# Kernel optimization log

Hardware: AMD Instinct MI355X
Metric: run time of the kernel (lower is better)

The kernel has to match this reference:

```python
import jax, jax.numpy as jnp
import numpy as np

H = 1024      # hidden_size
V = 32000     # output_size (vocab)
L = 512       # max_length (encoder positions)
B = 256       # batch


def setup_inputs() -> dict:
    key = jax.random.key(0)
    ks = jax.random.split(key, 12)
    s = 0.02
    return {
        "input": jax.random.randint(ks[0], (B,), 0, V),
        "hidden": jax.random.normal(ks[1], (1, B, H), jnp.float32),
        "encoder_outputs": jax.random.normal(ks[2], (L, H), jnp.float32),
        # learned params (PyTorch layout: Linear weight is [out, in])
        "emb": jax.random.normal(ks[3], (V, H), jnp.float32) * s,
        "attn_W": jax.random.normal(ks[4], (L, 2 * H), jnp.float32) * s,
        "attn_b": jnp.zeros((L,), jnp.float32),
        "comb_W": jax.random.normal(ks[5], (H, 2 * H), jnp.float32) * s,
        "comb_b": jnp.zeros((H,), jnp.float32),
        "W_ih": jax.random.normal(ks[6], (3 * H, H), jnp.float32) * s,
        "W_hh": jax.random.normal(ks[7], (3 * H, H), jnp.float32) * s,
        "b_ih": jnp.zeros((3 * H,), jnp.float32),
        "b_hh": jnp.zeros((3 * H,), jnp.float32),
        "out_W": jax.random.normal(ks[8], (V, H), jnp.float32) * s,
        "out_b": jnp.zeros((V,), jnp.float32),
    }


def reference(input, hidden, encoder_outputs, emb, attn_W, attn_b,
              comb_W, comb_b, W_ih, W_hh, b_ih, b_hh, out_W, out_b):
    h = hidden[0]                                   # [B,H]
    embedded = emb[input]                           # [B,H] (dropout in eval mode = identity)
    attn_logits = jnp.concatenate([embedded, h], axis=1) @ attn_W.T + attn_b
    attn_weights = jax.nn.softmax(attn_logits, axis=1)        # [B,L]
    attn_applied = attn_weights @ encoder_outputs              # [B,H]
    x = jnp.concatenate([embedded, attn_applied], axis=1) @ comb_W.T + comb_b
    x = jax.nn.relu(x)                                         # [B,H]
    # single-step GRU (PyTorch gate layout: r, z, n)
    gi = x @ W_ih.T + b_ih                                     # [B,3H]
    gh = h @ W_hh.T + b_hh                                     # [B,3H]
    gi_r, gi_z, gi_n = jnp.split(gi, 3, axis=1)
    gh_r, gh_z, gh_n = jnp.split(gh, 3, axis=1)
    r = jax.nn.sigmoid(gi_r + gh_r)
    z = jax.nn.sigmoid(gi_z + gh_z)
    n = jnp.tanh(gi_n + r * gh_n)
    h_new = (1.0 - z) * n + z * h                              # [B,H]
    output = jax.nn.log_softmax(h_new @ out_W.T + out_b, axis=1)  # [B,V]
    return output, h_new[None], attn_weights
```

## Files before the change

kernel.cpp:

```cpp
#include <hip/hip_runtime.h>
#include <hip/hip_bf16.h>
#include <cstdint>

#define DEVI __device__ __forceinline__

typedef __bf16 bf16x8 __attribute__((ext_vector_type(8)));
typedef float  f32x4  __attribute__((ext_vector_type(4)));

constexpr int Hdim = 1024;
constexpr int Vdim = 32000;
constexpr int Ldim = 512;
constexpr int Bdim = 256;

DEVI unsigned short f2bf(float f) {
  __bf16 h = (__bf16)f;
  return __builtin_bit_cast(unsigned short, h);
}

template<int WM, bool ABF16, bool DUAL>
__global__ __launch_bounds__(256, 2)
void gemm_bt(const void* __restrict__ Av0, const float* __restrict__ Wt0,
             const void* __restrict__ Av1, const float* __restrict__ Wt1,
             const float* __restrict__ bias,
             float* __restrict__ C0, float* __restrict__ C1,
             int K, int ldc, int col_off, int act, int aact0,
             int nsplit, float2* __restrict__ plse)
{
  constexpr int MT    = 4 * WM;
  constexpr int PITCH = 40;
  constexpr int ITA   = MT / 32;
  constexpr int MR    = WM / 16;

  __shared__ unsigned short lA[2 * MT * PITCH];
  __shared__ unsigned short lW[2 * 64 * PITCH];

  const int t  = threadIdx.x;
  const int m0 = blockIdx.y * MT;
  const int n0 = blockIdx.x * 64;

  int kz = blockIdx.z, half = 0;
  if (DUAL) { half = (kz >= nsplit) ? 1 : 0; kz -= half * nsplit; }
  const int NK = K / (32 * nsplit);
  const int kb = kz * NK;

  const void*  Av = (DUAL && half) ? Av1 : Av0;
  const float* Wt = (DUAL && half) ? Wt1 : Wt0;
  float*       C  = (DUAL && half) ? C1  : C0;
  const int  aact = (DUAL && half) ? 0 : aact0;

  const int tr = t >> 3;
  const int tc = (t & 7) * 4;

  const float*          Af = ABF16 ? nullptr : ((const float*)Av) + (size_t)m0 * K;
  const unsigned short* Ab = ABF16 ? ((const unsigned short*)Av) + (size_t)m0 * K : nullptr;
  const float*          Wb = Wt + (size_t)n0 * K;

  const int lane = t & 63;
  const int wv   = t >> 6;
  const int r16  = lane & 15;
  const int k8   = (lane >> 4) * 8;

  f32x4 acc[MR][4];
#pragma unroll
  for (int m = 0; m < MR; ++m)
#pragma unroll
    for (int n = 0; n < 4; ++n)
#pragma unroll
      for (int r = 0; r < 4; ++r) acc[m][n][r] = 0.f;

  struct RS { f32x4 ra[ITA]; ushort4 rab[ITA]; f32x4 rw[2]; };

  auto loadT = [&](RS& rg, int kt) {
    const int ko = (kb + kt) * 32 + tc;
    if constexpr (ABF16) {
      const unsigned short* ap = Ab + ko;
#pragma unroll
      for (int i = 0; i < ITA; ++i)
        rg.rab[i] = *reinterpret_cast<const ushort4*>(ap + (size_t)(tr + 32 * i) * K);
    } else {
      const float* ap = Af + ko;
#pragma unroll
      for (int i = 0; i < ITA; ++i)
        rg.ra[i] = *reinterpret_cast<const f32x4*>(ap + (size_t)(tr + 32 * i) * K);
    }
    const float* wp = Wb + ko;
#pragma unroll
    for (int i = 0; i < 2; ++i)
      rg.rw[i] = *reinterpret_cast<const f32x4*>(wp + (size_t)(tr + 32 * i) * K);
  };

  auto storeT = [&](RS& rg, int bo) {
    unsigned short* sA = &lA[bo * MT * PITCH];
    unsigned short* sW = &lW[bo * 64 * PITCH];
#pragma unroll
    for (int i = 0; i < ITA; ++i) {
      ushort4 u;
      if constexpr (ABF16) u = rg.rab[i];
      else {
        f32x4 v = rg.ra[i];
        if (aact) { v[0]=fmaxf(v[0],0.f); v[1]=fmaxf(v[1],0.f);
                    v[2]=fmaxf(v[2],0.f); v[3]=fmaxf(v[3],0.f); }
        u.x = f2bf(v[0]); u.y = f2bf(v[1]); u.z = f2bf(v[2]); u.w = f2bf(v[3]);
      }
      *reinterpret_cast<ushort4*>(&sA[(tr + 32 * i) * PITCH + tc]) = u;
    }
#pragma unroll
    for (int i = 0; i < 2; ++i) {
      f32x4 v = rg.rw[i]; ushort4 u;
      u.x = f2bf(v[0]); u.y = f2bf(v[1]); u.z = f2bf(v[2]); u.w = f2bf(v[3]);
      *reinterpret_cast<ushort4*>(&sW[(tr + 32 * i) * PITCH + tc]) = u;
    }
  };

  auto comp = [&](int bo) {
    const unsigned short* sA = &lA[bo * MT * PITCH];
    const unsigned short* sW = &lW[bo * 64 * PITCH];
    bf16x8 af[MR], bfr[4];
#pragma unroll
    for (int m = 0; m < MR; ++m)
      af[m] = *reinterpret_cast<const bf16x8*>(&sA[(wv * WM + m * 16 + r16) * PITCH + k8]);
#pragma unroll
    for (int n = 0; n < 4; ++n)
      bfr[n] = *reinterpret_cast<const bf16x8*>(&sW[(n * 16 + r16) * PITCH + k8]);
#pragma unroll
    for (int m = 0; m < MR; ++m)
#pragma unroll
      for (int n = 0; n < 4; ++n)
        acc[m][n] = __builtin_amdgcn_mfma_f32_16x16x32_bf16(af[m], bfr[n], acc[m][n], 0, 0, 0);
  };

#define GB_BARRIER() do { \
    asm volatile("s_waitcnt lgkmcnt(0)" ::: "memory"); \
    __builtin_amdgcn_sched_barrier(0); \
    __builtin_amdgcn_s_barrier(); \
  } while (0)

  RS ra_, rb_;
  loadT(ra_, 0);
  loadT(rb_, 1);
  storeT(ra_, 0);
  GB_BARRIER();

  for (int kt = 0; kt < NK; kt += 2) {
    if (kt + 2 < NK) loadT(ra_, kt + 2);
    comp(0);
    storeT(rb_, 1);
    GB_BARRIER();
    if (kt + 3 < NK) loadT(rb_, kt + 3);
    comp(1);
    if (kt + 2 < NK) {
      storeT(ra_, 0);
      GB_BARRIER();
    }
  }
#undef GB_BARRIER

#pragma unroll
  for (int n = 0; n < 4; ++n) {
    const int col = n0 + n * 16 + r16;
    const float bv = (bias && nsplit == 1) ? bias[col] : 0.f;
#pragma unroll
    for (int m = 0; m < MR; ++m) {
      const int rbase = m0 + wv * WM + m * 16 + (lane >> 4) * 4;
#pragma unroll
      for (int r = 0; r < 4; ++r) {
        float v = acc[m][n][r] + bv;
        if (act) v = fmaxf(v, 0.f);
        if (nsplit > 1) {
          atomicAdd(&C[(size_t)(rbase + r) * ldc + col_off + col], v);
        } else {
          C[(size_t)(rbase + r) * ldc + col_off + col] = v;
          acc[m][n][r] = v;
        }
      }
    }
  }

  if (plse) {
#pragma unroll
    for (int m = 0; m < MR; ++m) {
#pragma unroll
      for (int r = 0; r < 4; ++r) {
        float mx = fmaxf(fmaxf(acc[m][0][r], acc[m][1][r]),
                         fmaxf(acc[m][2][r], acc[m][3][r]));
#pragma unroll
        for (int o = 1; o < 16; o <<= 1) mx = fmaxf(mx, __shfl_xor(mx, o, 16));
        float s = 0.f;
#pragma unroll
        for (int n = 0; n < 4; ++n) s += __expf(acc[m][n][r] - mx);
#pragma unroll
        for (int o = 1; o < 16; o <<= 1) s += __shfl_xor(s, o, 16);
        if (r16 == 0) {
          const int row = m0 + wv * WM + m * 16 + (lane >> 4) * 4 + r;
          plse[(size_t)row * gridDim.x + blockIdx.x] = make_float2(mx, s);
        }
      }
    }
  }
}

__global__ void prep_kernel(const int* __restrict__ ids, const float* __restrict__ hid,
                            const float* __restrict__ emb,
                            const float* __restrict__ attn_b, const float* __restrict__ comb_b,
                            const float* __restrict__ b_ih, const float* __restrict__ b_hh,
                            float* __restrict__ X0, float* __restrict__ X1,
                            float* __restrict__ alog, float* __restrict__ xact,
                            float* __restrict__ gi, float* __restrict__ gh)
{
  const int b = blockIdx.x, t = threadIdx.x;
  const int row = ids[b];
  f32x4 e = *reinterpret_cast<const f32x4*>(emb + (size_t)row * Hdim + t * 4);
  *reinterpret_cast<f32x4*>(X0 + (size_t)b * 2048 + t * 4) = e;
  *reinterpret_cast<f32x4*>(X1 + (size_t)b * 2048 + t * 4) = e;
  f32x4 h = *reinterpret_cast<const f32x4*>(hid + (size_t)b * Hdim + t * 4);
  *reinterpret_cast<f32x4*>(X0 + (size_t)b * 2048 + 1024 + t * 4) = h;
  f32x4 z4 = {0.f, 0.f, 0.f, 0.f};
  *reinterpret_cast<f32x4*>(X1 + (size_t)b * 2048 + 1024 + t * 4) = z4;
  if (t < 128)
    *reinterpret_cast<f32x4*>(alog + (size_t)b * Ldim + t * 4) =
        *reinterpret_cast<const f32x4*>(attn_b + t * 4);
  *reinterpret_cast<f32x4*>(xact + (size_t)b * Hdim + t * 4) =
      *reinterpret_cast<const f32x4*>(comb_b + t * 4);
#pragma unroll
  for (int i = 0; i < 3; ++i) {
    *reinterpret_cast<f32x4*>(gi + (size_t)b * 3072 + i * 1024 + t * 4) =
        *reinterpret_cast<const f32x4*>(b_ih + i * 1024 + t * 4);
    *reinterpret_cast<f32x4*>(gh + (size_t)b * 3072 + i * 1024 + t * 4) =
        *reinterpret_cast<const f32x4*>(b_hh + i * 1024 + t * 4);
  }
}

__global__ void transpose_kernel(const float* __restrict__ enc, float* __restrict__ encT)
{
  __shared__ float tile[64][65];
  const int l0 = blockIdx.x * 64, h0 = blockIdx.y * 64;
  const int t = threadIdx.x;
  const int c = t & 63, rr = t >> 6;
#pragma unroll
  for (int p = 0; p < 16; ++p) {
    const int r = p * 4 + rr;
    tile[r][c] = enc[(size_t)(l0 + r) * Hdim + h0 + c];
  }
  __syncthreads();
#pragma unroll
  for (int p = 0; p < 16; ++p) {
    const int r = p * 4 + rr;
    encT[(size_t)(h0 + r) * Ldim + l0 + c] = tile[c][r];
  }
}

__global__ void attn_softmax_kernel(const float* __restrict__ logits, float* __restrict__ wout)
{
  __shared__ float red[256];
  const int b = blockIdx.x, t = threadIdx.x;
  const float x0 = logits[b * Ldim + t];
  const float x1 = logits[b * Ldim + 256 + t];
  red[t] = fmaxf(x0, x1); __syncthreads();
  for (int o = 128; o > 0; o >>= 1) { if (t < o) red[t] = fmaxf(red[t], red[t + o]); __syncthreads(); }
  const float m = red[0]; __syncthreads();
  const float e0 = __expf(x0 - m), e1 = __expf(x1 - m);
  red[t] = e0 + e1; __syncthreads();
  for (int o = 128; o > 0; o >>= 1) { if (t < o) red[t] += red[t + o]; __syncthreads(); }
  const float inv = 1.f / red[0];
  wout[b * Ldim + t]       = e0 * inv;
  wout[b * Ldim + 256 + t] = e1 * inv;
}

DEVI float sigm(float x) { return 1.f / (1.f + __expf(-x)); }

__global__ void gru_kernel(const float* __restrict__ gi, const float* __restrict__ gh,
                           const float* __restrict__ hin,
                           float* __restrict__ hnew, unsigned short* __restrict__ hnbf)
{
  const int idx = blockIdx.x * 256 + threadIdx.x;
  const int b = idx >> 10, j = idx & 1023;
  const float* gib = gi + (size_t)b * 3072;
  const float* ghb = gh + (size_t)b * 3072;
  const float r = sigm(gib[j] + ghb[j]);
  const float z = sigm(gib[1024 + j] + ghb[1024 + j]);
  const float n = tanhf(gib[2048 + j] + r * ghb[2048 + j]);
  const float h = hin[idx];
  const float hn = (1.f - z) * n + z * h;
  hnew[idx] = hn;
  hnbf[idx] = f2bf(hn);
}

__global__ void lsm_final(const float2* __restrict__ part, int npart, float* __restrict__ out)
{
  __shared__ float rm[256], rs[256];
  const int b = blockIdx.x, t = threadIdx.x;
  float m = -1e30f, s = 0.f;
  for (int j = t; j < npart; j += 256) {
    const float2 p = part[(size_t)b * npart + j];
    const float nm = fmaxf(m, p.x);
    s = s * __expf(m - nm) + p.y * __expf(p.x - nm);
    m = nm;
  }
  rm[t] = m; rs[t] = s; __syncthreads();
  for (int o = 128; o > 0; o >>= 1) {
    if (t < o) {
      const float m2 = rm[t + o], s2 = rs[t + o];
      const float nm = fmaxf(rm[t], m2);
      rs[t] = rs[t] * __expf(rm[t] - nm) + s2 * __expf(m2 - nm);
      rm[t] = nm;
    }
    __syncthreads();
  }
  const float lse = rm[0] + __logf(rs[0]);
  f32x4* row4 = reinterpret_cast<f32x4*>(out + (size_t)b * Vdim);
  for (int i = t; i < Vdim / 4; i += 256) {
    f32x4 x = row4[i];
    x[0] -= lse; x[1] -= lse; x[2] -= lse; x[3] -= lse;
    row4[i] = x;
  }
}

extern "C" void kernel_launch(void* const* d_in, const int* in_sizes, int n_in,
                              void* d_out, int out_size, void* d_ws, size_t ws_size,
                              hipStream_t stream)
{
  (void)in_sizes; (void)n_in; (void)out_size; (void)ws_size;

  const int*   ids    = (const int*)  d_in[0];
  const float* hid    = (const float*)d_in[1];
  const float* enc    = (const float*)d_in[2];
  const float* emb    = (const float*)d_in[3];
  const float* attn_W = (const float*)d_in[4];
  const float* attn_b = (const float*)d_in[5];
  const float* comb_W = (const float*)d_in[6];
  const float* comb_b = (const float*)d_in[7];
  const float* W_ih   = (const float*)d_in[8];
  const float* W_hh   = (const float*)d_in[9];
  const float* b_ih   = (const float*)d_in[10];
  const float* b_hh   = (const float*)d_in[11];
  const float* out_W  = (const float*)d_in[12];
  const float* out_b  = (const float*)d_in[13];

  float* out_logits = (float*)d_out;
  float* out_h      = out_logits + (size_t)Bdim * Vdim;
  float* out_attw   = out_h + (size_t)Bdim * Hdim;

  char* w = (char*)d_ws;
  float* X0   = (float*)w; w += (size_t)Bdim * 2048 * 4;
  float* X1   = (float*)w; w += (size_t)Bdim * 2048 * 4;
  float* encT = (float*)w; w += (size_t)Hdim * Ldim * 4;
  float* alog = (float*)w; w += (size_t)Bdim * Ldim * 4;
  float* xact = (float*)w; w += (size_t)Bdim * Hdim * 4;
  float* gi   = (float*)w; w += (size_t)Bdim * 3 * Hdim * 4;
  float* gh   = (float*)w; w += (size_t)Bdim * 3 * Hdim * 4;
  unsigned short* hnbf = (unsigned short*)w; w += (size_t)Bdim * Hdim * 2;
  float2* plse = (float2*)w; w += (size_t)Bdim * (Vdim / 64) * 8;

  prep_kernel<<<Bdim, 256, 0, stream>>>(ids, hid, emb, attn_b, comb_b, b_ih, b_hh,
                                        X0, X1, alog, xact, gi, gh);
  transpose_kernel<<<dim3(Ldim / 64, Hdim / 64), 256, 0, stream>>>(enc, encT);

  gemm_bt<32, false, false><<<dim3(Ldim / 64, 2, 8), 256, 0, stream>>>(
      X0, attn_W, nullptr, nullptr, nullptr, alog, nullptr,
      2048, Ldim, 0, 0, 0, 8, nullptr);
  attn_softmax_kernel<<<Bdim, 256, 0, stream>>>(alog, out_attw);

  gemm_bt<32, false, false><<<dim3(Hdim / 64, 2, 4), 256, 0, stream>>>(
      out_attw, encT, nullptr, nullptr, nullptr, X1, nullptr,
      512, 2048, 1024, 0, 0, 4, nullptr);

  gemm_bt<32, false, false><<<dim3(Hdim / 64, 2, 8), 256, 0, stream>>>(
      X1, comb_W, nullptr, nullptr, nullptr, xact, nullptr,
      2048, Hdim, 0, 0, 0, 8, nullptr);

  gemm_bt<32, false, true><<<dim3(3 * Hdim / 64, 2, 8), 256, 0, stream>>>(
      xact, W_ih, hid, W_hh, nullptr, gi, gh,
      1024, 3 * Hdim, 0, 0, 1, 4, nullptr);

  gru_kernel<<<Bdim * Hdim / 256, 256, 0, stream>>>(gi, gh, hid, out_h, hnbf);

  gemm_bt<64, true, false><<<dim3(Vdim / 64, 1, 1), 256, 0, stream>>>(
      hnbf, out_W, nullptr, nullptr, out_b, out_logits, nullptr,
      1024, Vdim, 0, 0, 0, 1, plse);

  lsm_final<<<Bdim, 256, 0, stream>>>(plse, Vdim / 64, out_logits);
}
```

Before: 129.7 us.

## Add dedicated pipelined vocab GEMM and split log-softmax finalization

Replaces the generic bt GEMM for the vocab projection with a specialized kernel. The new kernel keeps bf16 A fragments in registers straight from global memory and streams fp32 W tiles into a 4-deep LDS ring using global_load_lds with an XOR swizzle, with explicit waitcnt and barrier scheduling. It also splits the final log-softmax into a per-row LSE reduction and a wider 2048-block subtraction pass, so the bandwidth-bound pass uses more of the GPU. The cost is hand-tuned scheduling code, an extra kernel launch, and removal of the plse path from the generic GEMM.

```diff
diff --git a/kernel.cpp b/kernel.cpp
--- a/kernel.cpp
+++ b/kernel.cpp
@@ -15,6 +15,150 @@
 DEVI unsigned short f2bf(float f) {
   __bf16 h = (__bf16)f;
   return __builtin_bit_cast(unsigned short, h);
+}
+
+DEVI void load_lds16(const void* g, void* l) {
+  __builtin_amdgcn_global_load_lds(
+      (const __attribute__((address_space(1))) unsigned int*)g,
+      (__attribute__((address_space(3))) unsigned int*)l, 16, 0, 0);
+}
+
+constexpr int GF_NKT = 32;
+
+__global__ __launch_bounds__(256, 2)
+void gemm_flat(const unsigned short* __restrict__ A,
+               const float* __restrict__ W,
+               const float* __restrict__ bias,
+               float* __restrict__ C,
+               float2* __restrict__ plse)
+{
+  __shared__ float lW[4][64 * 32];
+
+  const int t    = threadIdx.x;
+  const int lane = t & 63;
+  const int wv   = t >> 6;
+  const int r16  = lane & 15;
+  const int k8   = (lane >> 4) * 8;
+  const int s0   = (lane >> 4) * 2;
+  const int n0   = blockIdx.x * 64;
+  const int drow0 = wv * 16 + (lane >> 3);
+
+  uint4 aset[4][4];
+  f32x4 acc[4][4];
+#pragma unroll
+  for (int m = 0; m < 4; ++m)
+#pragma unroll
+    for (int n = 0; n < 4; ++n)
+#pragma unroll
+      for (int r = 0; r < 4; ++r) acc[m][n][r] = 0.f;
+
+#define ISSUE_A(SET, KT) do {                                                  \
+    const int ko_ = (KT) * 32 + k8;                                            \
+    _Pragma("unroll")                                                          \
+    for (int m = 0; m < 4; ++m)                                                \
+      aset[SET][m] = *reinterpret_cast<const uint4*>(                          \
+          A + (size_t)(wv * 64 + m * 16 + r16) * 1024 + ko_);                  \
+  } while (0)
+
+#define ISSUE_W(BUF, KT) do {                                                  \
+    _Pragma("unroll")                                                          \
+    for (int q = 0; q < 2; ++q) {                                              \
+      const int row_ = drow0 + q * 8;                                          \
+      const float* src_ = W + (size_t)(n0 + row_) * 1024 + (KT) * 32           \
+                          + (((lane & 7) ^ (row_ & 7)) * 4);                   \
+      load_lds16(src_, &lW[BUF][(wv * 2 + q) * 256]);                          \
+    }                                                                          \
+  } while (0)
+
+#define STEP_COMPUTE(P) do {                                                   \
+    bf16x8 bw[4];                                                              \
+    _Pragma("unroll")                                                          \
+    for (int n = 0; n < 4; ++n) {                                              \
+      const int row_ = n * 16 + r16;                                           \
+      const int sw_  = row_ & 7;                                               \
+      f32x4 w0 = *reinterpret_cast<const f32x4*>(                              \
+          &lW[P][row_ * 32 + ((s0 ^ sw_) * 4)]);                               \
+      f32x4 w1 = *reinterpret_cast<const f32x4*>(                              \
+          &lW[P][row_ * 32 + (((s0 + 1) ^ sw_) * 4)]);                         \
+      bf16x8 v;                                                                \
+      v[0] = (__bf16)w0[0]; v[1] = (__bf16)w0[1];                              \
+      v[2] = (__bf16)w0[2]; v[3] = (__bf16)w0[3];                              \
+      v[4] = (__bf16)w1[0]; v[5] = (__bf16)w1[1];                              \
+      v[6] = (__bf16)w1[2]; v[7] = (__bf16)w1[3];                              \
+      bw[n] = v;                                                               \
+    }                                                                          \
+    _Pragma("unroll")                                                          \
+    for (int m = 0; m < 4; ++m) {                                              \
+      bf16x8 am = __builtin_bit_cast(bf16x8, aset[P][m]);                      \
+      _Pragma("unroll")                                                        \
+      for (int n = 0; n < 4; ++n)                                              \
+        acc[m][n] = __builtin_amdgcn_mfma_f32_16x16x32_bf16(am, bw[n],         \
+                                                            acc[m][n], 0,0,0);\
+    }                                                                          \
+  } while (0)
+
+#define STEP(P, I) do {                                                        \
+    asm volatile("s_waitcnt vmcnt(12)" ::: "memory");                          \
+    __builtin_amdgcn_sched_barrier(0);                                         \
+    __builtin_amdgcn_s_barrier();                                              \
+    __builtin_amdgcn_sched_barrier(0);                                         \
+    { const int kn_ = ((I) + 3 < GF_NKT) ? (I) + 3 : GF_NKT - 1;               \
+      ISSUE_A((P + 3) & 3, kn_); ISSUE_W((P + 3) & 3, kn_); }                  \
+    __builtin_amdgcn_sched_barrier(0);                                         \
+    STEP_COMPUTE(P);                                                           \
+    __builtin_amdgcn_sched_barrier(0);                                         \
+  } while (0)
+
+  ISSUE_A(0, 0); ISSUE_W(0, 0);
+  ISSUE_A(1, 1); ISSUE_W(1, 1);
+  ISSUE_A(2, 2); ISSUE_W(2, 2);
+
+  for (int ib = 0; ib < GF_NKT; ib += 4) {
+    STEP(0, ib);
+    STEP(1, ib + 1);
+    STEP(2, ib + 2);
+    STEP(3, ib + 3);
+  }
+
+#undef STEP
+#undef STEP_COMPUTE
+#undef ISSUE_W
+#undef ISSUE_A
+
+#pragma unroll
+  for (int n = 0; n < 4; ++n) {
+    const int col = n0 + n * 16 + r16;
+    const float bv = bias[col];
+#pragma unroll
+    for (int m = 0; m < 4; ++m) {
+      const int rbase = wv * 64 + m * 16 + (lane >> 4) * 4;
+#pragma unroll
+      for (int r = 0; r < 4; ++r) {
+        const float v = acc[m][n][r] + bv;
+        acc[m][n][r] = v;
+        C[(size_t)(rbase + r) * Vdim + col] = v;
+      }
+    }
+  }
+#pragma unroll
+  for (int m = 0; m < 4; ++m) {
+#pragma unroll
+    for (int r = 0; r < 4; ++r) {
+      float mx = fmaxf(fmaxf(acc[m][0][r], acc[m][1][r]),
+                       fmaxf(acc[m][2][r], acc[m][3][r]));
+#pragma unroll
+      for (int o = 1; o < 16; o <<= 1) mx = fmaxf(mx, __shfl_xor(mx, o, 16));
+      float s = 0.f;
+#pragma unroll
+      for (int n = 0; n < 4; ++n) s += __expf(acc[m][n][r] - mx);
+#pragma unroll
+      for (int o = 1; o < 16; o <<= 1) s += __shfl_xor(s, o, 16);
+      if (r16 == 0) {
+        const int row = wv * 64 + m * 16 + (lane >> 4) * 4 + r;
+        plse[(size_t)row * gridDim.x + blockIdx.x] = make_float2(mx, s);
+      }
+    }
+  }
 }
 
 template<int WM, bool ABF16, bool DUAL>
@@ -24,7 +168,7 @@
              const float* __restrict__ bias,
              float* __restrict__ C0, float* __restrict__ C1,
              int K, int ldc, int col_off, int act, int aact0,
-             int nsplit, float2* __restrict__ plse)
+             int nsplit)
 {
   constexpr int MT    = 4 * WM;
   constexpr int PITCH = 40;
@@ -170,29 +314,6 @@
           atomicAdd(&C[(size_t)(rbase + r) * ldc + col_off + col], v);
         } else {
           C[(size_t)(rbase + r) * ldc + col_off + col] = v;
-          acc[m][n][r] = v;
-        }
-      }
-    }
-  }
-
-  if (plse) {
-#pragma unroll
-    for (int m = 0; m < MR; ++m) {
-#pragma unroll
-      for (int r = 0; r < 4; ++r) {
-        float mx = fmaxf(fmaxf(acc[m][0][r], acc[m][1][r]),
-                         fmaxf(acc[m][2][r], acc[m][3][r]));
-#pragma unroll
-        for (int o = 1; o < 16; o <<= 1) mx = fmaxf(mx, __shfl_xor(mx, o, 16));
-        float s = 0.f;
-#pragma unroll
-        for (int n = 0; n < 4; ++n) s += __expf(acc[m][n][r] - mx);
-#pragma unroll
-        for (int o = 1; o < 16; o <<= 1) s += __shfl_xor(s, o, 16);
-        if (r16 == 0) {
-          const int row = m0 + wv * WM + m * 16 + (lane >> 4) * 4 + r;
-          plse[(size_t)row * gridDim.x + blockIdx.x] = make_float2(mx, s);
         }
       }
     }
@@ -285,7 +406,8 @@
   hnbf[idx] = f2bf(hn);
 }
 
-__global__ void lsm_final(const float2* __restrict__ part, int npart, float* __restrict__ out)
+__global__ void lse_reduce(const float2* __restrict__ part, int npart,
+                           float* __restrict__ lse)
 {
   __shared__ float rm[256], rs[256];
   const int b = blockIdx.x, t = threadIdx.x;
@@ -306,11 +428,17 @@
     }
     __syncthreads();
   }
-  const float lse = rm[0] + __logf(rs[0]);
-  f32x4* row4 = reinterpret_cast<f32x4*>(out + (size_t)b * Vdim);
-  for (int i = t; i < Vdim / 4; i += 256) {
+  if (t == 0) lse[b] = rm[0] + __logf(rs[0]);
+}
+
+__global__ void lsm_sub(const float* __restrict__ lse, float* __restrict__ out)
+{
+  const int b = blockIdx.x >> 3, c = blockIdx.x & 7;
+  const float l = lse[b];
+  f32x4* row4 = reinterpret_cast<f32x4*>(out + (size_t)b * Vdim) + c * 1000;
+  for (int i = threadIdx.x; i < 1000; i += 256) {
     f32x4 x = row4[i];
-    x[0] -= lse; x[1] -= lse; x[2] -= lse; x[3] -= lse;
+    x[0] -= l; x[1] -= l; x[2] -= l; x[3] -= l;
     row4[i] = x;
   }
 }
@@ -350,6 +478,7 @@
   float* gh   = (float*)w; w += (size_t)Bdim * 3 * Hdim * 4;
   unsigned short* hnbf = (unsigned short*)w; w += (size_t)Bdim * Hdim * 2;
   float2* plse = (float2*)w; w += (size_t)Bdim * (Vdim / 64) * 8;
+  float* lse  = (float*)w; w += (size_t)Bdim * 4;
 
   prep_kernel<<<Bdim, 256, 0, stream>>>(ids, hid, emb, attn_b, comb_b, b_ih, b_hh,
                                         X0, X1, alog, xact, gi, gh);
@@ -357,26 +486,25 @@
 
   gemm_bt<32, false, false><<<dim3(Ldim / 64, 2, 8), 256, 0, stream>>>(
       X0, attn_W, nullptr, nullptr, nullptr, alog, nullptr,
-      2048, Ldim, 0, 0, 0, 8, nullptr);
+      2048, Ldim, 0, 0, 0, 8);
   attn_softmax_kernel<<<Bdim, 256, 0, stream>>>(alog, out_attw);
 
   gemm_bt<32, false, false><<<dim3(Hdim / 64, 2, 4), 256, 0, stream>>>(
       out_attw, encT, nullptr, nullptr, nullptr, X1, nullptr,
-      512, 2048, 1024, 0, 0, 4, nullptr);
+      512, 2048, 1024, 0, 0, 4);
 
   gemm_bt<32, false, false><<<dim3(Hdim / 64, 2, 8), 256, 0, stream>>>(
       X1, comb_W, nullptr, nullptr, nullptr, xact, nullptr,
-      2048, Hdim, 0, 0, 0, 8, nullptr);
+      2048, Hdim, 0, 0, 0, 8);
 
   gemm_bt<32, false, true><<<dim3(3 * Hdim / 64, 2, 8), 256, 0, stream>>>(
       xact, W_ih, hid, W_hh, nullptr, gi, gh,
-      1024, 3 * Hdim, 0, 0, 1, 4, nullptr);
+      1024, 3 * Hdim, 0, 0, 1, 4);
 
   gru_kernel<<<Bdim * Hdim / 256, 256, 0, stream>>>(gi, gh, hid, out_h, hnbf);
 
-  gemm_bt<64, true, false><<<dim3(Vdim / 64, 1, 1), 256, 0, stream>>>(
-      hnbf, out_W, nullptr, nullptr, out_b, out_logits, nullptr,
-      1024, Vdim, 0, 0, 0, 1, plse);
-
-  lsm_final<<<Bdim, 256, 0, stream>>>(plse, Vdim / 64, out_logits);
-}
+  gemm_flat<<<Vdim / 64, 256, 0, stream>>>(hnbf, out_W, out_b, out_logits, plse);
+
+  lse_reduce<<<Bdim, 256, 0, stream>>>(plse, Vdim / 64, lse);
+  lsm_sub<<<Bdim * 8, 256, 0, stream>>>(lse, out_logits);
+}
```

Result: slower. 138.0 us (+6.4%).
